# Kernel optimization log

Measured on AMD Instinct MI355X. Metric: run time of the kernel, lower is better.

## Reference

```python
import jax, jax.numpy as jnp
import numpy as np

DIM = 384
HEADS = 12
WIN = (2, 7, 7)
MLP_RATIO = 4.0
EPS = 1e-5


def _rel_index(Wt, Wh, Ww):
    t, h, w = np.meshgrid(np.arange(Wt), np.arange(Wh), np.arange(Ww), indexing='ij')
    coords = np.stack([t, h, w]).reshape(3, -1).T  # (N,3)
    rel = coords[:, None] - coords[None]  # (N,N,3)
    rel[..., 0] += Wt - 1
    rel[..., 1] += Wh - 1
    rel[..., 2] += Ww - 1
    rel[..., 0] *= (2 * Wh - 1) * (2 * Ww - 1)
    rel[..., 1] *= (2 * Ww - 1)
    return rel.sum(-1)  # (N,N) int


def setup_inputs() -> dict:
    key = jax.random.key(0)
    ks = jax.random.split(key, 16)
    d = DIM
    hdim = int(d * MLP_RATIO)
    Wt, Wh, Ww = WIN
    table_size = (2 * Wt - 1) * (2 * Wh - 1) * (2 * Ww - 1)
    s = lambda fan: 1.0 / np.sqrt(fan)
    return {
        'x': jax.random.normal(ks[0], (2, 8, 56, 56, d), jnp.float32),
        'norm1_g': jnp.ones((d,), jnp.float32),
        'norm1_b': jnp.zeros((d,), jnp.float32),
        'qkv_w': jax.random.normal(ks[1], (d, 3 * d), jnp.float32) * s(d),
        'qkv_b': jnp.zeros((3 * d,), jnp.float32),
        'proj_w': jax.random.normal(ks[2], (d, d), jnp.float32) * s(d),
        'proj_b': jnp.zeros((d,), jnp.float32),
        'bias_table': jax.random.normal(ks[3], (table_size, HEADS), jnp.float32) * 0.02,
        'norm2_g': jnp.ones((d,), jnp.float32),
        'norm2_b': jnp.zeros((d,), jnp.float32),
        'fc1_w': jax.random.normal(ks[4], (d, hdim), jnp.float32) * s(d),
        'fc1_b': jnp.zeros((hdim,), jnp.float32),
        'fc2_w': jax.random.normal(ks[5], (hdim, d), jnp.float32) * s(hdim),
        'fc2_b': jnp.zeros((d,), jnp.float32),
        'rel_index': jnp.asarray(_rel_index(*WIN), jnp.int32),
    }


def _ln(x, g, b):
    mu = x.mean(-1, keepdims=True)
    var = ((x - mu) ** 2).mean(-1, keepdims=True)
    return (x - mu) * jax.lax.rsqrt(var + EPS) * g + b


def _window_partition(x, win):
    B, T, H, W, C = x.shape
    Wt, Wh, Ww = win
    x = x.reshape(B, T // Wt, Wt, H // Wh, Wh, W // Ww, Ww, C)
    x = x.transpose(0, 1, 3, 5, 2, 4, 6, 7)
    return x.reshape(-1, Wt * Wh * Ww, C)


def _window_reverse(win_x, win, B, T, H, W):
    Wt, Wh, Ww = win
    C = win_x.shape[-1]
    x = win_x.reshape(B, T // Wt, H // Wh, W // Ww, Wt, Wh, Ww, C)
    x = x.transpose(0, 1, 4, 2, 5, 3, 6, 7)
    return x.reshape(B, T, H, W, C)


def reference(x, norm1_g, norm1_b, qkv_w, qkv_b, proj_w, proj_b, bias_table,
              norm2_g, norm2_b, fc1_w, fc1_b, fc2_w, fc2_b, rel_index):
    B, T, H, W, C = x.shape
    Wt, Wh, Ww = WIN
    N = Wt * Wh * Ww
    shift = (Wt // 2, Wh // 2, Ww // 2)
    head_dim = C // HEADS
    scale = head_dim ** -0.5

    shortcut = x
    h = _ln(x, norm1_g, norm1_b)
    h = jnp.roll(h, shift=(-shift[0], -shift[1], -shift[2]), axis=(1, 2, 3))
    # dims chosen divisible by window -> no padding branch
    wins = _window_partition(h, WIN)  # (BnW, N, C)
    BnW = wins.shape[0]

    qkv = wins @ qkv_w + qkv_b  # (BnW, N, 3C)
    qkv = qkv.reshape(BnW, N, 3, HEADS, head_dim).transpose(2, 0, 3, 1, 4)
    q, k, v = qkv[0] * scale, qkv[1], qkv[2]  # (BnW, H, N, d)

    bias = bias_table[rel_index.reshape(-1)].reshape(N, N, HEADS).transpose(2, 0, 1)
    attn = jnp.einsum('bhnd,bhmd->bhnm', q, k) + bias[None]
    attn = jax.nn.softmax(attn, axis=-1)
    out = jnp.einsum('bhnm,bhmd->bhnd', attn, v)
    out = out.transpose(0, 2, 1, 3).reshape(BnW, N, C)
    out = out @ proj_w + proj_b

    h = _window_reverse(out.reshape(-1, Wt, Wh, Ww, C), WIN, B, T, H, W)
    h = jnp.roll(h, shift=shift, axis=(1, 2, 3))
    x = shortcut + h

    h2 = _ln(x, norm2_g, norm2_b)
    h2 = jax.nn.gelu(h2 @ fc1_w + fc1_b, approximate=False) @ fc2_w + fc2_b
    return x + h2
```

## Files before the change

### kernel.cpp

```cpp
#include <hip/hip_runtime.h>
#include <cstdint>
#include <cstddef>


typedef __bf16 bf16x8 __attribute__((ext_vector_type(8)));
typedef float f32x4 __attribute__((ext_vector_type(4)));

#define DIM 384
#define QKV_DIM 1152
#define HID 1536
#define NHEADS 12
#define NTOK 50176
#define NWIN 512

__device__ __forceinline__ void gload16(const void* g, void* s) {
  __builtin_amdgcn_global_load_lds(
      (const __attribute__((address_space(1))) void*)g,
      (__attribute__((address_space(3))) void*)s, 16, 0, 0);
}

__global__ __launch_bounds__(256) void build_tokmap_k(int* __restrict__ map) {
  int t = blockIdx.x * 256 + threadIdx.x;
  if (t >= NTOK) return;
  int win = t / 98, n = t - win * 98;
  int b = win >> 8, tw = (win >> 6) & 3, hw = (win >> 3) & 7, ww = win & 7;
  int dt = n / 49; int rem = n - dt * 49; int dh = rem / 7, dw = rem - dh * 7;
  int t0 = (tw * 2 + dt + 1) & 7;
  int h0 = hw * 7 + dh + 3; if (h0 >= 56) h0 -= 56;
  int w0 = ww * 7 + dw + 3; if (w0 >= 56) w0 -= 56;
  map[t] = ((b * 8 + t0) * 56 + h0) * 56 + w0;
}

__global__ __launch_bounds__(256) void expand_biasp_k(const float* __restrict__ table,
                                                      const int* __restrict__ rel,
                                                      float* __restrict__ out) {
  int e = blockIdx.x * 256 + threadIdx.x;
  if (e >= NHEADS * 49 * 256) return;
  int r = e & 3, l = (e >> 2) & 63;
  int rest = e >> 8;
  int ni = rest % 7, mi = (rest / 7) % 7, h = rest / 49;
  int i = mi * 16 + (l >> 4) * 4 + r;
  int j = ni * 16 + (l & 15);
  float v;
  if (j >= 98) v = -1e30f;
  else if (i >= 98) v = 0.f;
  else v = table[rel[i * 98 + j] * NHEADS + h];
  out[e] = v;
}

__global__ __launch_bounds__(256) void transpose_w_k(const float* __restrict__ W,
                                                     __bf16* __restrict__ WT,
                                                     int K, int N, int scaleCols, float scale) {
  int e = blockIdx.x * 256 + threadIdx.x;
  if (e >= K * N) return;
  int n = e / K, k = e - n * K;
  float v = W[(size_t)k * N + n];
  if (n < scaleCols) v *= scale;
  WT[e] = (__bf16)v;
}

__global__ __launch_bounds__(256) void scale_bias_k(const float* __restrict__ b,
                                                    float* __restrict__ out,
                                                    int n, int scaleCols, float scale) {
  int e = blockIdx.x * 256 + threadIdx.x;
  if (e >= n) return;
  out[e] = b[e] * (e < scaleCols ? scale : 1.0f);
}

__global__ __launch_bounds__(384) void vtrans_k(const __bf16* __restrict__ qkv,
                                                __bf16* __restrict__ vt) {
  int win = blockIdx.x, t = threadIdx.x;
  const __bf16* base = qkv + (size_t)win * 98 * QKV_DIM + 768 + t;
  __bf16* orow = vt + ((size_t)win * 384 + t) * 128;
  #pragma unroll
  for (int c = 0; c < 16; ++c) {
    bf16x8 pk;
    #pragma unroll
    for (int e2 = 0; e2 < 8; ++e2) {
      int tok = c * 8 + e2;
      pk[e2] = (tok < 98) ? base[(size_t)tok * QKV_DIM] : (__bf16)0.f;
    }
    *(bf16x8*)(orow + c * 8) = pk;
  }
}

__global__ __launch_bounds__(256) void ln_k(const float* __restrict__ x,
                                            const float* __restrict__ g,
                                            const float* __restrict__ bta,
                                            __bf16* __restrict__ out,
                                            const int* __restrict__ map) {
  int w = threadIdx.x >> 6, l = threadIdx.x & 63;
  int tok = blockIdx.x * 4 + w;
  int src = map ? map[tok] : tok;
  const float* row = x + (size_t)src * DIM;
  float v[6]; float s = 0.f;
  #pragma unroll
  for (int j = 0; j < 6; ++j) { v[j] = row[l + 64 * j]; s += v[j]; }
  #pragma unroll
  for (int m = 1; m < 64; m <<= 1) s += __shfl_xor(s, m, 64);
  float mu = s * (1.f / DIM);
  float var = 0.f;
  #pragma unroll
  for (int j = 0; j < 6; ++j) { float d = v[j] - mu; var += d * d; }
  #pragma unroll
  for (int m = 1; m < 64; m <<= 1) var += __shfl_xor(var, m, 64);
  float rs = rsqrtf(var * (1.f / DIM) + 1e-5f);
  __bf16* orow = out + (size_t)tok * DIM;
  #pragma unroll
  for (int j = 0; j < 6; ++j) {
    int c = l + 64 * j;
    orow[c] = (__bf16)((v[j] - mu) * rs * g[c] + bta[c]);
  }
}

template <int EPI>
__global__ __launch_bounds__(256) void gemm_k(const __bf16* __restrict__ A,
                                              const __bf16* __restrict__ BT,
                                              const float* __restrict__ bias,
                                              int M, int N, int K,
                                              __bf16* __restrict__ outb,
                                              float* __restrict__ outf,
                                              const float* __restrict__ resid,
                                              const int* __restrict__ tokmap) {
  __shared__ __align__(1024) char sA[16384];
  __shared__ __align__(1024) char sB[16384];
  const int tid = threadIdx.x;
  const int l = tid & 63, w = tid >> 6;
  const int lr = l & 15, lg = l >> 4;
  const int ntile = N >> 7;
  const int nwg8 = gridDim.x >> 3;
  const int bid = (blockIdx.x & 7) * nwg8 + (blockIdx.x >> 3);
  const int bm = bid / ntile, bn = bid - bm * ntile;
  const int m0 = bm << 7, n0 = bn << 7;
  const int wr = w >> 1, wc = w & 1;
  const int srow = l >> 3;
  const int sch = (l & 7) ^ srow;
  const __bf16* pa = A + (size_t)(m0 + w * 32 + srow) * K + sch * 8;
  const __bf16* pb = BT + (size_t)(n0 + w * 32 + srow) * K + sch * 8;
  char* dA = sA + w * 32 * 128;
  char* dB = sB + w * 32 * 128;

  f32x4 acc[4][4] = {};
  const int nk = K >> 6;
  for (int kt = 0; kt < nk; ++kt) {
    const int koff = kt << 6;
    __syncthreads();
    #pragma unroll
    for (int i = 0; i < 4; ++i) {
      gload16(pa + (size_t)(i * 8) * K + koff, dA + i * 1024);
      gload16(pb + (size_t)(i * 8) * K + koff, dB + i * 1024);
    }
    __syncthreads();
    #pragma unroll
    for (int kk = 0; kk < 2; ++kk) {
      bf16x8 af[4], bfv[4];
      const int ck = (kk << 2) + lg;
      #pragma unroll
      for (int m = 0; m < 4; ++m) {
        int r = (wr << 6) + (m << 4) + lr;
        af[m] = *(const bf16x8*)(sA + (r << 7) + ((ck ^ (r & 7)) << 4));
      }
      #pragma unroll
      for (int n = 0; n < 4; ++n) {
        int r = (wc << 6) + (n << 4) + lr;
        bfv[n] = *(const bf16x8*)(sB + (r << 7) + ((ck ^ (r & 7)) << 4));
      }
      #pragma unroll
      for (int m = 0; m < 4; ++m)
        #pragma unroll
        for (int n = 0; n < 4; ++n)
          acc[m][n] = __builtin_amdgcn_mfma_f32_16x16x32_bf16(af[m], bfv[n], acc[m][n], 0, 0, 0);
    }
  }
  #pragma unroll
  for (int m = 0; m < 4; ++m) {
    int gm0 = m0 + (wr << 6) + (m << 4) + (lg << 2);
    #pragma unroll
    for (int n = 0; n < 4; ++n) {
      int gn = n0 + (wc << 6) + (n << 4) + lr;
      f32x4 a = acc[m][n];
      float bb = bias[gn];
      if (EPI == 0) {
        #pragma unroll
        for (int r = 0; r < 4; ++r)
          outb[(size_t)(gm0 + r) * N + gn] = (__bf16)(a[r] + bb);
      } else if (EPI == 1) {
        #pragma unroll
        for (int r = 0; r < 4; ++r) {
          int dst = tokmap[gm0 + r];
          size_t idx = (size_t)dst * DIM + gn;
          outf[idx] = resid[idx] + a[r] + bb;
        }
      } else if (EPI == 2) {
        #pragma unroll
        for (int r = 0; r < 4; ++r) {
          float vv = a[r] + bb;
          float y = vv * (1.0f + 0.044715f * vv * vv);
          outb[(size_t)(gm0 + r) * N + gn] =
              (__bf16)(vv / (1.0f + __expf(-1.5957691216057308f * y)));
        }
      } else {
        #pragma unroll
        for (int r = 0; r < 4; ++r) {
          size_t idx = (size_t)(gm0 + r) * N + gn;
          outf[idx] = resid[idx] + a[r] + bb;
        }
      }
    }
  }
}

__global__ __launch_bounds__(64) void attn_k(const __bf16* __restrict__ qkv,
                                             const __bf16* __restrict__ vt,
                                             const float* __restrict__ pb,
                                             __bf16* __restrict__ out) {
  __shared__ __align__(1024) char P[4096];
  const int l = threadIdx.x, lr = l & 15, lg = l >> 4;
  const int bid = blockIdx.x;
  const int xc = bid & 7, kk = bid >> 3;
  const int wh = (kk / 7) * 8 + xc, mi = kk % 7;
  const int win = wh / NHEADS, h = wh - win * NHEADS;
  const size_t wbase = (size_t)win * 98 * QKV_DIM;
  const __bf16* qb = qkv + wbase + h * 32;
  const __bf16* kb = qb + 384;
  const bf16x8 z8 = {};
  const f32x4 fz = {};

  bf16x8 kf[7];
  #pragma unroll
  for (int ni = 0; ni < 7; ++ni) {
    int tok = ni * 16 + lr;
    kf[ni] = (tok < 98) ? *(const bf16x8*)(kb + (size_t)tok * QKV_DIM + lg * 8) : z8;
  }
  int qt = mi * 16 + lr;
  bf16x8 qf = (qt < 98) ? *(const bf16x8*)(qb + (size_t)qt * QKV_DIM + lg * 8) : z8;
  const f32x4* pbp = (const f32x4*)pb + (size_t)((h * 7 + mi) * 7) * 64 + l;
  f32x4 bv[7];
  #pragma unroll
  for (int ni = 0; ni < 7; ++ni) bv[ni] = pbp[ni * 64];

  f32x4 s[7];
  #pragma unroll
  for (int ni = 0; ni < 7; ++ni)
    s[ni] = __builtin_amdgcn_mfma_f32_16x16x32_bf16(qf, kf[ni], fz, 0, 0, 0);

  if (l < 32) {
    int row = l >> 1, c = 14 + (l & 1);
    *(f32x4*)(P + row * 256 + ((c ^ (row & 7)) << 4)) = fz;
  }

  #pragma unroll
  for (int r = 0; r < 4; ++r) {
    float mx = -1e30f;
    #pragma unroll
    for (int ni = 0; ni < 7; ++ni) {
      float vv = s[ni][r] + bv[ni][r];
      s[ni][r] = vv;
      mx = fmaxf(mx, vv);
    }
    #pragma unroll
    for (int m2 = 1; m2 < 16; m2 <<= 1) mx = fmaxf(mx, __shfl_xor(mx, m2, 64));
    float sum = 0.f;
    #pragma unroll
    for (int ni = 0; ni < 7; ++ni) { float p = __expf(s[ni][r] - mx); s[ni][r] = p; sum += p; }
    #pragma unroll
    for (int m2 = 1; m2 < 16; m2 <<= 1) sum += __shfl_xor(sum, m2, 64);
    float inv = 1.0f / sum;
    int il = lg * 4 + r;
    #pragma unroll
    for (int ni = 0; ni < 7; ++ni) {
      int j = ni * 16 + lr;
      *(__bf16*)(P + il * 256 + (((j >> 3) ^ (il & 7)) << 4) + ((j & 7) << 1)) =
          (__bf16)(s[ni][r] * inv);
    }
  }
  __syncthreads();

  bf16x8 pa[4];
  #pragma unroll
  for (int ks = 0; ks < 4; ++ks) {
    int ck = ks * 4 + lg;
    pa[ks] = *(const bf16x8*)(P + lr * 256 + ((ck ^ (lr & 7)) << 4));
  }
  const __bf16* vrow = vt + ((size_t)wh * 32) * 128;
  __bf16* ob = out + ((size_t)win * 98 + mi * 16) * DIM + h * 32;
  #pragma unroll
  for (int nf = 0; nf < 2; ++nf) {
    int d = nf * 16 + lr;
    f32x4 o = fz;
    #pragma unroll
    for (int ks = 0; ks < 4; ++ks) {
      bf16x8 vb = *(const bf16x8*)(vrow + (size_t)d * 128 + ks * 32 + lg * 8);
      o = __builtin_amdgcn_mfma_f32_16x16x32_bf16(pa[ks], vb, o, 0, 0, 0);
    }
    #pragma unroll
    for (int r = 0; r < 4; ++r) {
      int il = lg * 4 + r;
      if (mi * 16 + il < 98) ob[(size_t)il * DIM + nf * 16 + lr] = (__bf16)o[r];
    }
  }
}

extern "C" void kernel_launch(void* const* d_in, const int* in_sizes, int n_in,
                              void* d_out, int out_size, void* d_ws, size_t ws_size,
                              hipStream_t stream) {
  const float* x      = (const float*)d_in[0];
  const float* n1g    = (const float*)d_in[1];
  const float* n1b    = (const float*)d_in[2];
  const float* qkv_w  = (const float*)d_in[3];
  const float* qkv_b  = (const float*)d_in[4];
  const float* proj_w = (const float*)d_in[5];
  const float* proj_b = (const float*)d_in[6];
  const float* btab   = (const float*)d_in[7];
  const float* n2g    = (const float*)d_in[8];
  const float* n2b    = (const float*)d_in[9];
  const float* fc1_w  = (const float*)d_in[10];
  const float* fc1_b  = (const float*)d_in[11];
  const float* fc2_w  = (const float*)d_in[12];
  const float* fc2_b  = (const float*)d_in[13];
  const int*   relidx = (const int*)d_in[14];
  float* outp = (float*)d_out;
  (void)in_sizes; (void)n_in; (void)out_size; (void)ws_size;

  char* ws = (char*)d_ws;
  size_t off = 0;
  auto alloc = [&](size_t bytes) {
    char* p = ws + off;
    off = (off + bytes + 255) & ~(size_t)255;
    return p;
  };
  int*    tokmap = (int*)alloc((size_t)NTOK * 4);
  float*  biasex = (float*)alloc((size_t)NHEADS * 49 * 256 * 4);
  __bf16* wqkvT  = (__bf16*)alloc((size_t)QKV_DIM * DIM * 2);
  __bf16* wprojT = (__bf16*)alloc((size_t)DIM * DIM * 2);
  __bf16* wfc1T  = (__bf16*)alloc((size_t)HID * DIM * 2);
  __bf16* wfc2T  = (__bf16*)alloc((size_t)DIM * HID * 2);
  float*  qkvbS  = (float*)alloc((size_t)QKV_DIM * 4);
  __bf16* tokens = (__bf16*)alloc((size_t)NTOK * DIM * 2);
  __bf16* qkvbuf = (__bf16*)alloc((size_t)NTOK * HID * 2);
  __bf16* attnout = tokens;
  __bf16* h1 = qkvbuf;
  __bf16* vt = (__bf16*)d_out;

  const float scale = 0.17677669529663687f;

  build_tokmap_k<<<NTOK / 256, 256, 0, stream>>>(tokmap);
  expand_biasp_k<<<(NHEADS * 49 * 256) / 256, 256, 0, stream>>>(btab, relidx, biasex);
  transpose_w_k<<<(DIM * QKV_DIM) / 256, 256, 0, stream>>>(qkv_w, wqkvT, DIM, QKV_DIM, DIM, scale);
  transpose_w_k<<<(DIM * DIM) / 256, 256, 0, stream>>>(proj_w, wprojT, DIM, DIM, 0, 1.0f);
  transpose_w_k<<<(DIM * HID) / 256, 256, 0, stream>>>(fc1_w, wfc1T, DIM, HID, 0, 1.0f);
  transpose_w_k<<<(HID * DIM) / 256, 256, 0, stream>>>(fc2_w, wfc2T, HID, DIM, 0, 1.0f);
  scale_bias_k<<<(QKV_DIM + 255) / 256, 256, 0, stream>>>(qkv_b, qkvbS, QKV_DIM, DIM, scale);

  ln_k<<<NTOK / 4, 256, 0, stream>>>(x, n1g, n1b, tokens, tokmap);
  gemm_k<0><<<(NTOK / 128) * (QKV_DIM / 128), 256, 0, stream>>>(
      tokens, wqkvT, qkvbS, NTOK, QKV_DIM, DIM, qkvbuf, nullptr, nullptr, nullptr);
  vtrans_k<<<NWIN, 384, 0, stream>>>(qkvbuf, vt);
  attn_k<<<NWIN * NHEADS * 7, 64, 0, stream>>>(qkvbuf, vt, biasex, attnout);
  gemm_k<1><<<(NTOK / 128) * (DIM / 128), 256, 0, stream>>>(
      attnout, wprojT, proj_b, NTOK, DIM, DIM, nullptr, outp, x, tokmap);
  ln_k<<<NTOK / 4, 256, 0, stream>>>(outp, n2g, n2b, tokens, nullptr);
  gemm_k<2><<<(NTOK / 128) * (HID / 128), 256, 0, stream>>>(
      tokens, wfc1T, fc1_b, NTOK, HID, DIM, h1, nullptr, nullptr, nullptr);
  gemm_k<3><<<(NTOK / 128) * (DIM / 128), 256, 0, stream>>>(
      h1, wfc2T, fc2_b, NTOK, DIM, HID, nullptr, outp, outp, nullptr);
}
```

Measured before the change: 519.2 us.

## Double-buffer GEMM LDS tiles and vectorize epilogue via transposed MFMA

```diff
diff --git a/kernel.cpp b/kernel.cpp
--- a/kernel.cpp
+++ b/kernel.cpp
@@ -4,6 +4,7 @@
 
 
 typedef __bf16 bf16x8 __attribute__((ext_vector_type(8)));
+typedef __bf16 bf16x4 __attribute__((ext_vector_type(4)));
 typedef float f32x4 __attribute__((ext_vector_type(4)));
 
 #define DIM 384
@@ -122,8 +123,7 @@
                                               float* __restrict__ outf,
                                               const float* __restrict__ resid,
                                               const int* __restrict__ tokmap) {
-  __shared__ __align__(1024) char sA[16384];
-  __shared__ __align__(1024) char sB[16384];
+  __shared__ __align__(1024) char lds[65536];
   const int tid = threadIdx.x;
   const int l = tid & 63, w = tid >> 6;
   const int lr = l & 15, lg = l >> 4;
@@ -137,20 +137,31 @@
   const int sch = (l & 7) ^ srow;
   const __bf16* pa = A + (size_t)(m0 + w * 32 + srow) * K + sch * 8;
   const __bf16* pb = BT + (size_t)(n0 + w * 32 + srow) * K + sch * 8;
-  char* dA = sA + w * 32 * 128;
-  char* dB = sB + w * 32 * 128;
+  const int doff = w * 4096;
+  const int nk = K >> 6;
+
+  #pragma unroll
+  for (int i = 0; i < 4; ++i) {
+    gload16(pa + (size_t)(i * 8) * K, lds + doff + i * 1024);
+    gload16(pb + (size_t)(i * 8) * K, lds + 16384 + doff + i * 1024);
+  }
 
   f32x4 acc[4][4] = {};
-  const int nk = K >> 6;
   for (int kt = 0; kt < nk; ++kt) {
-    const int koff = kt << 6;
-    __syncthreads();
-    #pragma unroll
-    for (int i = 0; i < 4; ++i) {
-      gload16(pa + (size_t)(i * 8) * K + koff, dA + i * 1024);
-      gload16(pb + (size_t)(i * 8) * K + koff, dB + i * 1024);
-    }
-    __syncthreads();
+    char* cur = lds + ((kt & 1) << 15);
+    if (kt + 1 < nk) {
+      char* nxt = lds + (((kt + 1) & 1) << 15);
+      const size_t koff = (size_t)(kt + 1) << 6;
+      #pragma unroll
+      for (int i = 0; i < 4; ++i) {
+        gload16(pa + (size_t)(i * 8) * K + koff, nxt + doff + i * 1024);
+        gload16(pb + (size_t)(i * 8) * K + koff, nxt + 16384 + doff + i * 1024);
+      }
+      asm volatile("s_waitcnt vmcnt(8)" ::: "memory");
+    } else {
+      asm volatile("s_waitcnt vmcnt(0)" ::: "memory");
+    }
+    asm volatile("s_barrier" ::: "memory");
     #pragma unroll
     for (int kk = 0; kk < 2; ++kk) {
       bf16x8 af[4], bfv[4];
@@ -158,53 +169,50 @@
       #pragma unroll
       for (int m = 0; m < 4; ++m) {
         int r = (wr << 6) + (m << 4) + lr;
-        af[m] = *(const bf16x8*)(sA + (r << 7) + ((ck ^ (r & 7)) << 4));
+        af[m] = *(const bf16x8*)(cur + (r << 7) + ((ck ^ (r & 7)) << 4));
       }
       #pragma unroll
       for (int n = 0; n < 4; ++n) {
         int r = (wc << 6) + (n << 4) + lr;
-        bfv[n] = *(const bf16x8*)(sB + (r << 7) + ((ck ^ (r & 7)) << 4));
+        bfv[n] = *(const bf16x8*)(cur + 16384 + (r << 7) + ((ck ^ (r & 7)) << 4));
       }
       #pragma unroll
       for (int m = 0; m < 4; ++m)
         #pragma unroll
         for (int n = 0; n < 4; ++n)
-          acc[m][n] = __builtin_amdgcn_mfma_f32_16x16x32_bf16(af[m], bfv[n], acc[m][n], 0, 0, 0);
-    }
-  }
+          acc[m][n] = __builtin_amdgcn_mfma_f32_16x16x32_bf16(bfv[n], af[m], acc[m][n], 0, 0, 0);
+    }
+    asm volatile("s_barrier" ::: "memory");
+  }
+
   #pragma unroll
   for (int m = 0; m < 4; ++m) {
-    int gm0 = m0 + (wr << 6) + (m << 4) + (lg << 2);
+    const int grow = m0 + (wr << 6) + (m << 4) + lr;
     #pragma unroll
     for (int n = 0; n < 4; ++n) {
-      int gn = n0 + (wc << 6) + (n << 4) + lr;
-      f32x4 a = acc[m][n];
-      float bb = bias[gn];
+      const int gcol = n0 + (wc << 6) + (n << 4) + (lg << 2);
+      f32x4 a = acc[m][n] + *(const f32x4*)(bias + gcol);
       if (EPI == 0) {
+        bf16x4 c;
         #pragma unroll
-        for (int r = 0; r < 4; ++r)
-          outb[(size_t)(gm0 + r) * N + gn] = (__bf16)(a[r] + bb);
+        for (int r = 0; r < 4; ++r) c[r] = (__bf16)a[r];
+        *(bf16x4*)(outb + (size_t)grow * N + gcol) = c;
       } else if (EPI == 1) {
+        int dst = tokmap[grow];
+        f32x4 rv = *(const f32x4*)(resid + (size_t)dst * DIM + gcol);
+        *(f32x4*)(outf + (size_t)dst * DIM + gcol) = rv + a;
+      } else if (EPI == 2) {
+        bf16x4 c;
         #pragma unroll
         for (int r = 0; r < 4; ++r) {
-          int dst = tokmap[gm0 + r];
-          size_t idx = (size_t)dst * DIM + gn;
-          outf[idx] = resid[idx] + a[r] + bb;
+          float vv = a[r];
+          float y = vv * (1.0f + 0.044715f * vv * vv);
+          c[r] = (__bf16)(vv / (1.0f + __expf(-1.5957691216057308f * y)));
         }
-      } else if (EPI == 2) {
-        #pragma unroll
-        for (int r = 0; r < 4; ++r) {
-          float vv = a[r] + bb;
-          float y = vv * (1.0f + 0.044715f * vv * vv);
-          outb[(size_t)(gm0 + r) * N + gn] =
-              (__bf16)(vv / (1.0f + __expf(-1.5957691216057308f * y)));
-        }
+        *(bf16x4*)(outb + (size_t)grow * N + gcol) = c;
       } else {
-        #pragma unroll
-        for (int r = 0; r < 4; ++r) {
-          size_t idx = (size_t)(gm0 + r) * N + gn;
-          outf[idx] = resid[idx] + a[r] + bb;
-        }
+        f32x4 rv = *(const f32x4*)(resid + (size_t)grow * N + gcol);
+        *(f32x4*)(outf + (size_t)grow * N + gcol) = rv + a;
       }
     }
   }
```

Result: faster. 483.1 us (-6.9%).
